# Optimization experiments

Hardware: AMD Instinct MI355X
Metric: run time of the kernel (lower is better)

Reference implementation:

```python
import jax, jax.numpy as jnp
import numpy as np

VOCAB, ED, HW, HS, NC = 100000, 200, 100, 100, 10
B, S, W = 128, 40, 50


def setup_inputs() -> dict:
    key = jax.random.key(0)
    ks = jax.random.split(key, 24)
    def p(k, shape, s=0.05):
        return jax.random.normal(k, shape, dtype=jnp.float32) * s
    emb = p(ks[0], (VOCAB, ED)).at[VOCAB - 1].set(0.0)  # padding_idx = vocab-1
    d = dict(
        x=jax.random.randint(ks[23], (B, S, W), 0, VOCAB),
        emb=emb,
        # word bidirectional GRU (forward + backward cells), torch gate order r,z,n
        w_Wih_f=p(ks[1], (3 * HW, ED)), w_bih_f=p(ks[2], (3 * HW,)), w_bhh_f=p(ks[3], (3 * HW,)),
        w_Wih_b=p(ks[4], (3 * HW, ED)), w_bih_b=p(ks[5], (3 * HW,)), w_bhh_b=p(ks[6], (3 * HW,)),
        # word attention
        wa_W=p(ks[7], (2 * HW, 2 * HW)), wa_b=p(ks[8], (2 * HW,)), wa_ctx=p(ks[9], (2 * HW,)),
        # sentence bidirectional GRU (input = 2*HW)
        s_Wih_f=p(ks[10], (3 * HS, 2 * HW)), s_bih_f=p(ks[11], (3 * HS,)), s_bhh_f=p(ks[12], (3 * HS,)),
        s_Wih_b=p(ks[13], (3 * HS, 2 * HW)), s_bih_b=p(ks[14], (3 * HS,)), s_bhh_b=p(ks[15], (3 * HS,)),
        # sentence attention
        sa_W=p(ks[16], (2 * HS, 2 * HS)), sa_b=p(ks[17], (2 * HS,)), sa_ctx=p(ks[18], (2 * HS,)),
        # classifier
        fc_W=p(ks[19], (NC, 2 * HS)), fc_b=p(ks[20], (NC,)),
    )
    return d


def _gru0(x, Wih, bih, bhh, H):
    # GRU cell from zero hidden state: W_hh @ h0 == 0, only b_hh survives.
    g = x @ Wih.T + bih  # [..., 3H], gate order r, z, n
    r = jax.nn.sigmoid(g[..., :H] + bhh[:H])
    z = jax.nn.sigmoid(g[..., H:2 * H] + bhh[H:2 * H])
    n = jnp.tanh(g[..., 2 * H:] + r * bhh[2 * H:])
    return (1.0 - z) * n  # h' = (1-z)*n + z*0


def _bigru0(x, Wf, bf, bhf, Wb, bb, bhb, H):
    # one-timestep bidirectional GRU: fwd and bwd cells both see zero state
    return jnp.concatenate([_gru0(x, Wf, bf, bhf, H), _gru0(x, Wb, bb, bhb, H)], axis=-1)


def _attn(x, Wa, ba, ctx):
    # additive attention pooling over the second-to-last axis
    scores = jnp.einsum('...nd,d->...n', jnp.tanh(x @ Wa.T + ba), ctx)
    alpha = jax.nn.softmax(scores, axis=-1)
    return jnp.einsum('...n,...nd->...d', alpha, x)


def reference(x, emb, w_Wih_f, w_bih_f, w_bhh_f, w_Wih_b, w_bih_b, w_bhh_b,
              wa_W, wa_b, wa_ctx, s_Wih_f, s_bih_f, s_bhh_f, s_Wih_b, s_bih_b, s_bhh_b,
              sa_W, sa_b, sa_ctx, fc_W, fc_b):
    e = emb[x]                                                   # [B,S,W,ED]
    wenc = _bigru0(e, w_Wih_f, w_bih_f, w_bhh_f, w_Wih_b, w_bih_b, w_bhh_b, HW)  # [B,S,W,2HW]
    svec = _attn(wenc, wa_W, wa_b, wa_ctx)                       # [B,S,2HW]
    senc = _bigru0(svec, s_Wih_f, s_bih_f, s_bhh_f, s_Wih_b, s_bih_b, s_bhh_b, HS)  # [B,S,2HS]
    dvec = _attn(senc, sa_W, sa_b, sa_ctx)                       # [B,2HS]
    logits = dvec @ fc_W.T + fc_b                                # [B,NC]
    return jax.nn.log_softmax(logits, axis=1)
```

## Files before the change

### kernel.cpp

```cpp
#include <hip/hip_runtime.h>
#include <math.h>

#define NB    128
#define NS    40
#define NW    50
#define ED    200
#define NHW   100
#define FEAT  200
#define NC    10
#define VOCABM1 99999
#define KL2E  1.4426950408889634f

#define BBn      19712ull
#define OFF_SV   846336ull
#define OFF_DV   2894336ull
#define WS_NEED  4194304ull

#define SLOT   19712

typedef short bf16x8 __attribute__((ext_vector_type(8)));
typedef float f32x4  __attribute__((ext_vector_type(4)));
typedef unsigned u32x4 __attribute__((ext_vector_type(4)));

__device__ __forceinline__ unsigned short f2bf(float f) {
    unsigned int u = __float_as_uint(f);
    u += 0x7fffu + ((u >> 16) & 1u);
    return (unsigned short)(u >> 16);
}
__device__ __forceinline__ float bf2f(short s) {
    return __uint_as_float(((unsigned int)(unsigned short)s) << 16);
}
__device__ __forceinline__ unsigned pk2(float a, float b) {
    return (unsigned)f2bf(a) | ((unsigned)f2bf(b) << 16);
}
__device__ __forceinline__ float frcp(float x) { return __builtin_amdgcn_rcpf(x); }
#if __has_builtin(__builtin_amdgcn_exp2f)
__device__ __forceinline__ float fexp2(float x){ return __builtin_amdgcn_exp2f(x); }
#else
__device__ __forceinline__ float fexp2(float x){ return exp2f(x); }
#endif
__device__ __forceinline__ float fsig(float x) { return frcp(1.f + __expf(-x)); }
__device__ __forceinline__ float ftanh(float x){ return 1.f - 2.f*frcp(1.f + __expf(2.f*x)); }

__device__ __forceinline__ unsigned cvtpk(float lo, float hi) {
    unsigned r;
    asm("v_cvt_pk_bf16_f32 %0, %1, %2" : "=v"(r) : "v"(lo), "v"(hi));
    return r;
}
__device__ __forceinline__ bf16x8 pack8(float4 a, float4 b) {
    u32x4 t;
    t[0] = cvtpk(a.x, a.y); t[1] = cvtpk(a.z, a.w);
    t[2] = cvtpk(b.x, b.y); t[3] = cvtpk(b.z, b.w);
    return __builtin_bit_cast(bf16x8, t);
}

__device__ __forceinline__ void gld16(const void* g, void* l) {
    __builtin_amdgcn_global_load_lds(
        (const __attribute__((address_space(1))) void*)g,
        (__attribute__((address_space(3))) void*)l, 16, 0, 0);
}

__device__ __forceinline__ void stageBlob(char* __restrict__ dst,
                                          const char* __restrict__ src, int tid)
{
    #pragma unroll
    for (int u = 0; u < 4; ++u)
        gld16(src + (size_t)(u * 256 + tid) * 16, dst + (size_t)(u * 256 + tid) * 16);
    if (tid < 208)
        gld16(src + (size_t)(1024 + tid) * 16, dst + (size_t)(1024 + tid) * 16);
}

__global__ void pack_kernel(
    const float* __restrict__ wWf, const float* __restrict__ wbif, const float* __restrict__ wbhf,
    const float* __restrict__ wWb, const float* __restrict__ wbib, const float* __restrict__ wbhb,
    const float* __restrict__ waW, const float* __restrict__ wab, const float* __restrict__ wactx,
    const float* __restrict__ sWf, const float* __restrict__ sbif, const float* __restrict__ sbhf,
    const float* __restrict__ sWb, const float* __restrict__ sbib, const float* __restrict__ sbhb,
    const float* __restrict__ saW, const float* __restrict__ sab, const float* __restrict__ sactx,
    char* __restrict__ ws)
{
    const int b = blockIdx.x, tid = threadIdx.x;
    const bool word = b < 19;
    const int lb = word ? b : b - 19;
    char* blob = ws + (size_t)b * BBn;

    if (lb < 14) {
        const int s = lb;
        const float* Wf_ = word ? wWf : sWf;
        const float* Wb_ = word ? wWb : sWb;
        const float* bif = word ? wbif : sbif;
        const float* bhf = word ? wbhf : sbhf;
        const float* bib = word ? wbib : sbib;
        const float* bhb = word ? wbhb : sbhb;
        const int ub = (s >> 1) * 32 + (s & 1) * 4;

        for (int e = tid; e < 18 * 64; e += 256) {
            const int f = e >> 6, l = e & 63;
            const int gate = f % 3, kk = f / 3;
            const int i = l & 15;
            const int k0 = kk * 32 + (l >> 4) * 8;
            const int u = ub + ((i >> 2) << 3) + (i & 3);
            u32x4 out = {0u, 0u, 0u, 0u};
            if (u < 200) {
                const float* W = (u < 100) ? Wf_ : Wb_;
                const int j = (u < 100) ? u : u - 100;
                const float* src = W + (size_t)(gate * NHW + j) * ED + k0;
                out[0] = pk2(src[0], src[1]); out[1] = pk2(src[2], src[3]);
                out[2] = pk2(src[4], src[5]); out[3] = pk2(src[6], src[7]);
            }
            *(u32x4*)(blob + ((size_t)f << 10) + (size_t)l * 16) = out;
        }
        if (tid < 48) {
            const int gate = tid >> 4, i = tid & 15;
            const int u = ub + ((i >> 2) << 3) + (i & 3);
            u32x4 out = {0u, 0u, 0u, 0u};
            if (u < 200) {
                const float* W = (u < 100) ? Wf_ : Wb_;
                const int j = (u < 100) ? u : u - 100;
                const float* src = W + (size_t)(gate * NHW + j) * ED + 192;
                out[0] = pk2(src[0], src[1]); out[1] = pk2(src[2], src[3]);
                out[2] = pk2(src[4], src[5]); out[3] = pk2(src[6], src[7]);
            }
            *(u32x4*)(blob + 18432 + gate * 256 + i * 16) = out;
        }
        if (tid < 64) {
            const int sect = tid >> 4, i = tid & 15;
            const int u = ub + ((i >> 2) << 3) + (i & 3);
            float v = 0.f;
            if (u < 200) {
                const float* bih = (u < 100) ? bif : bib;
                const float* bhh = (u < 100) ? bhf : bhb;
                const int j = (u < 100) ? u : u - 100;
                if (sect == 0)      v = -KL2E * (bih[j] + bhh[j]);
                else if (sect == 1) v =  KL2E * (bih[NHW + j] + bhh[NHW + j]);
                else if (sect == 2) v = 2.f * KL2E * bih[2 * NHW + j];
                else                v = 2.f * KL2E * bhh[2 * NHW + j];
            }
            *(float*)(blob + 19200 + sect * 64 + i * 4) = v;
        }
    } else {
        const int cb = lb - 14;
        const float* W  = word ? waW : saW;
        const float* ab = word ? wab : sab;
        const float* cx = word ? wactx : sactx;
        for (int e = tid; e < 18 * 64; e += 256) {
            const int f = e >> 6, l = e & 63;
            const int g = f % 3, kk = f / 3;
            const int d = cb * 48 + g * 16 + (l & 15);
            const int k0 = kk * 32 + (l >> 4) * 8;
            u32x4 out = {0u, 0u, 0u, 0u};
            if (d < FEAT) {
                const float* src = W + (size_t)d * FEAT + k0;
                out[0] = pk2(src[0], src[1]); out[1] = pk2(src[2], src[3]);
                out[2] = pk2(src[4], src[5]); out[3] = pk2(src[6], src[7]);
            }
            *(u32x4*)(blob + ((size_t)f << 10) + (size_t)l * 16) = out;
        }
        if (tid < 48) {
            const int g = tid >> 4, i = tid & 15;
            const int d = cb * 48 + g * 16 + i;
            u32x4 out = {0u, 0u, 0u, 0u};
            if (d < FEAT) {
                const float* src = W + (size_t)d * FEAT + 192;
                out[0] = pk2(src[0], src[1]); out[1] = pk2(src[2], src[3]);
                out[2] = pk2(src[4], src[5]); out[3] = pk2(src[6], src[7]);
            }
            *(u32x4*)(blob + 18432 + g * 256 + i * 16) = out;
        }
        if (tid < 48) {
            const int d = cb * 48 + tid;
            float ab2 = 0.f, cxn = 0.f;
            if (d < FEAT) { ab2 = 2.f * KL2E * ab[d]; cxn = -2.f * cx[d]; }
            *(float*)(blob + 19200 + tid * 4) = ab2;
            *(float*)(blob + 19392 + tid * 4) = cxn;
        }
    }
}

template<bool WORD>
__global__ __launch_bounds__(256, 3) void han_kernel(
    const int* __restrict__ xtok,
    const void* __restrict__ Ain,
    const char* __restrict__ pk,
    const int nvalid,
    unsigned short* __restrict__ Out)
{
    __shared__ __align__(16) char smem[2 * SLOT];
    char* bufs = smem;

    const int tid  = threadIdx.x;
    const int lane = tid & 63, wv = tid >> 6;
    const int grp  = wv >> 1, half = wv & 1;
    const int ln15 = lane & 15, q = lane >> 4;
    const long g   = (long)blockIdx.x * 2 + grp;
    float* sc_sh = (float*)(bufs + grp * 4096);
    float* al_sh = (float*)(bufs + grp * 4096 + 256);
    float* part  = (float*)(bufs + grp * 4096 + 512);

    stageBlob(bufs, pk, tid);

    bf16x8 af[2][7];
    if (WORD) {
        const float* emb = (const float*)Ain;
        #pragma unroll
        for (int Mt = 0; Mt < 2; ++Mt) {
            const int item = half * 32 + Mt * 16 + ln15;
            int tok = VOCABM1;
            if (item < nvalid) tok = xtok[g * nvalid + item];
            const float4* rp = (const float4*)(emb + (long)tok * ED);
            #pragma unroll
            for (int kc = 0; kc < 6; ++kc)
                af[Mt][kc] = pack8(rp[kc * 8 + q * 2], rp[kc * 8 + q * 2 + 1]);
            af[Mt][6] = (q == 0) ? pack8(rp[48], rp[49]) : (bf16x8)(short)0;
        }
    } else {
        const char* sv = (const char*)Ain;
        #pragma unroll
        for (int Mt = 0; Mt < 2; ++Mt) {
            const int item = half * 32 + Mt * 16 + ln15;
            const int ic = item < nvalid ? item : nvalid - 1;
            const char* rp = sv + (g * nvalid + ic) * 400;
            #pragma unroll
            for (int kc = 0; kc < 7; ++kc) {
                bf16x8 v = (bf16x8)(short)0;
                if (item < nvalid && (kc < 6 || q == 0))
                    v = *(const bf16x8*)(rp + kc * 64 + q * 16);
                af[Mt][kc] = v;
            }
        }
    }

    __syncthreads();

    u32x4 hfw[2][7];

    #pragma unroll
    for (int s = 0; s < 14; ++s) {
        stageBlob(bufs + (size_t)((s + 1) & 1) * SLOT, pk + (size_t)(s + 1) * BBn, tid);
        const char* cur = bufs + (size_t)(s & 1) * SLOT;

        f32x4 a0[2] = {}, a1[2] = {}, a2[2] = {};
        #pragma unroll
        for (int kk = 0; kk < 7; ++kk) {
            bf16x8 b0, b1, b2;
            if (kk < 6) {
                b0 = *(const bf16x8*)(cur + ((kk * 3 + 0) << 10) + lane * 16);
                b1 = *(const bf16x8*)(cur + ((kk * 3 + 1) << 10) + lane * 16);
                b2 = *(const bf16x8*)(cur + ((kk * 3 + 2) << 10) + lane * 16);
            } else {
                b0 = *(const bf16x8*)(cur + 18432 +   0 + ln15 * 16);
                b1 = *(const bf16x8*)(cur + 18432 + 256 + ln15 * 16);
                b2 = *(const bf16x8*)(cur + 18432 + 512 + ln15 * 16);
            }
            #pragma unroll
            for (int Mt = 0; Mt < 2; ++Mt) {
                a0[Mt] = __builtin_amdgcn_mfma_f32_16x16x32_bf16(b0, af[Mt][kk], a0[Mt], 0, 0, 0);
                a1[Mt] = __builtin_amdgcn_mfma_f32_16x16x32_bf16(b1, af[Mt][kk], a1[Mt], 0, 0, 0);
                a2[Mt] = __builtin_amdgcn_mfma_f32_16x16x32_bf16(b2, af[Mt][kk], a2[Mt], 0, 0, 0);
            }
        }
        const f32x4 bR = *(const f32x4*)(cur + 19200 +   0 + q * 16);
        const f32x4 bZ = *(const f32x4*)(cur + 19200 +  64 + q * 16);
        const f32x4 bN = *(const f32x4*)(cur + 19200 + 128 + q * 16);
        const f32x4 hN = *(const f32x4*)(cur + 19200 + 192 + q * 16);
        #pragma unroll
        for (int Mt = 0; Mt < 2; ++Mt) {
            float h[4];
            #pragma unroll
            for (int rg = 0; rg < 4; ++rg) {
                const float r  = frcp(1.f + fexp2(fmaf(a0[Mt][rg], -KL2E, bR[rg])));
                const float zc = frcp(1.f + fexp2(fmaf(a1[Mt][rg],  KL2E, bZ[rg])));
                const float t  = frcp(1.f + fexp2(fmaf(a2[Mt][rg], 2.f * KL2E,
                                          fmaf(r, hN[rg], bN[rg]))));
                h[rg] = zc * (1.f - 2.f * t);
            }
            hfw[Mt][s >> 1][(s & 1) * 2 + 0] = cvtpk(h[0], h[1]);
            hfw[Mt][s >> 1][(s & 1) * 2 + 1] = cvtpk(h[2], h[3]);
        }
        __syncthreads();
    }

    float sacc[2][4] = {{0.f}};
    #pragma unroll
    for (int s = 14; s < 19; ++s) {
        if (s + 1 < 19)
            stageBlob(bufs + (size_t)((s + 1) & 1) * SLOT, pk + (size_t)(s + 1) * BBn, tid);
        const char* cur = bufs + (size_t)(s & 1) * SLOT;

        f32x4 ac[2][3] = {};
        #pragma unroll
        for (int kk = 0; kk < 7; ++kk) {
            bf16x8 b0, b1, b2;
            if (kk < 6) {
                b0 = *(const bf16x8*)(cur + ((kk * 3 + 0) << 10) + lane * 16);
                b1 = *(const bf16x8*)(cur + ((kk * 3 + 1) << 10) + lane * 16);
                b2 = *(const bf16x8*)(cur + ((kk * 3 + 2) << 10) + lane * 16);
            } else {
                b0 = *(const bf16x8*)(cur + 18432 +   0 + ln15 * 16);
                b1 = *(const bf16x8*)(cur + 18432 + 256 + ln15 * 16);
                b2 = *(const bf16x8*)(cur + 18432 + 512 + ln15 * 16);
            }
            #pragma unroll
            for (int Mt = 0; Mt < 2; ++Mt) {
                const bf16x8 hfv = __builtin_bit_cast(bf16x8, hfw[Mt][kk]);
                ac[Mt][0] = __builtin_amdgcn_mfma_f32_16x16x32_bf16(hfv, b0, ac[Mt][0], 0, 0, 0);
                ac[Mt][1] = __builtin_amdgcn_mfma_f32_16x16x32_bf16(hfv, b1, ac[Mt][1], 0, 0, 0);
                ac[Mt][2] = __builtin_amdgcn_mfma_f32_16x16x32_bf16(hfv, b2, ac[Mt][2], 0, 0, 0);
            }
        }
        #pragma unroll
        for (int Nt = 0; Nt < 3; ++Nt) {
            const float ab2 = *(const float*)(cur + 19200 + (Nt * 16 + ln15) * 4);
            const float cxn = *(const float*)(cur + 19392 + (Nt * 16 + ln15) * 4);
            #pragma unroll
            for (int Mt = 0; Mt < 2; ++Mt)
                #pragma unroll
                for (int rg = 0; rg < 4; ++rg) {
                    const float u = frcp(1.f + fexp2(fmaf(ac[Mt][Nt][rg], 2.f * KL2E, ab2)));
                    sacc[Mt][rg] = fmaf(u, cxn, sacc[Mt][rg]);
                }
        }
        __syncthreads();
    }

    #pragma unroll
    for (int Mt = 0; Mt < 2; ++Mt)
        #pragma unroll
        for (int rg = 0; rg < 4; ++rg) {
            float v = sacc[Mt][rg];
            v += __shfl_xor(v, 1); v += __shfl_xor(v, 2);
            v += __shfl_xor(v, 4); v += __shfl_xor(v, 8);
            sacc[Mt][rg] = v;
        }
    if (ln15 == 0) {
        #pragma unroll
        for (int Mt = 0; Mt < 2; ++Mt)
            #pragma unroll
            for (int rg = 0; rg < 4; ++rg)
                sc_sh[half * 32 + Mt * 16 + q * 4 + rg] = sacc[Mt][rg];
    }
    __syncthreads();

    {
        const float sv0 = (lane < nvalid) ? sc_sh[lane] : -1e30f;
        float m = sv0;
        m = fmaxf(m, __shfl_xor(m, 1));  m = fmaxf(m, __shfl_xor(m, 2));
        m = fmaxf(m, __shfl_xor(m, 4));  m = fmaxf(m, __shfl_xor(m, 8));
        m = fmaxf(m, __shfl_xor(m, 16)); m = fmaxf(m, __shfl_xor(m, 32));
        const float e = (lane < nvalid) ? fexp2((sv0 - m) * KL2E) : 0.f;
        float ss = e;
        ss += __shfl_xor(ss, 1);  ss += __shfl_xor(ss, 2);
        ss += __shfl_xor(ss, 4);  ss += __shfl_xor(ss, 8);
        ss += __shfl_xor(ss, 16); ss += __shfl_xor(ss, 32);
        if (half == 0) al_sh[lane] = e * frcp(ss);
    }
    __syncthreads();

    {
        const float aM0 = al_sh[half * 32 + ln15];
        const float aM1 = al_sh[half * 32 + 16 + ln15];
        #pragma unroll
        for (int kc = 0; kc < 7; ++kc) {
            const bf16x8 h0 = __builtin_bit_cast(bf16x8, hfw[0][kc]);
            const bf16x8 h1 = __builtin_bit_cast(bf16x8, hfw[1][kc]);
            float p[8];
            #pragma unroll
            for (int j = 0; j < 8; ++j)
                p[j] = aM0 * bf2f(h0[j]) + aM1 * bf2f(h1[j]);
            #pragma unroll
            for (int j = 0; j < 8; ++j) {
                p[j] += __shfl_xor(p[j], 1); p[j] += __shfl_xor(p[j], 2);
                p[j] += __shfl_xor(p[j], 4); p[j] += __shfl_xor(p[j], 8);
            }
            if (ln15 == 0) {
                float* dst = part + (size_t)half * 224 + kc * 32 + q * 8;
                f32x4 v0 = {p[0], p[1], p[2], p[3]};
                f32x4 v1 = {p[4], p[5], p[6], p[7]};
                *(f32x4*)dst = v0; *(f32x4*)(dst + 4) = v1;
            }
        }
    }
    __syncthreads();

    if (tid < 100) {
        const int sl = tid / 50, i = tid - sl * 50;
        const float* pa = (const float*)(bufs + (size_t)sl * 4096 + 512);
        const float* pb = pa + 224;
        uint2 o;
        o.x = cvtpk(pa[i * 4 + 0] + pb[i * 4 + 0], pa[i * 4 + 1] + pb[i * 4 + 1]);
        o.y = cvtpk(pa[i * 4 + 2] + pb[i * 4 + 2], pa[i * 4 + 3] + pb[i * 4 + 3]);
        *(uint2*)(Out + ((long)blockIdx.x * 2 + sl) * 200 + i * 4) = o;
    }
}

__global__ void cls_kernel(const unsigned short* __restrict__ dvec,
                           const float* __restrict__ fcW, const float* __restrict__ fcb,
                           float* __restrict__ out)
{
    const int doc = blockIdx.x, lane = threadIdx.x;
    const int c = lane & 15, part = lane >> 4;
    const int cs = (c < NC) ? c : 0;
    float acc = (part == 0 && c < NC) ? fcb[c] : 0.f;
    for (int i = 0; i < 50; ++i) {
        const int k = part * 50 + i;
        const float a = bf2f((short)dvec[(size_t)doc * 200 + k]);
        acc += a * ((c < NC) ? fcW[(size_t)cs * 200 + k] : 0.f);
    }
    acc += __shfl_xor(acc, 16); acc += __shfl_xor(acc, 32);
    const float lg = (c < NC) ? acc : -1e30f;
    float m = lg;
    m = fmaxf(m, __shfl_xor(m, 1)); m = fmaxf(m, __shfl_xor(m, 2));
    m = fmaxf(m, __shfl_xor(m, 4)); m = fmaxf(m, __shfl_xor(m, 8));
    const float e = (c < NC) ? __expf(lg - m) : 0.f;
    float ss = e;
    ss += __shfl_xor(ss, 1); ss += __shfl_xor(ss, 2);
    ss += __shfl_xor(ss, 4); ss += __shfl_xor(ss, 8);
    const float lse = m + __logf(ss);
    if (lane < NC) out[(size_t)doc * NC + lane] = lg - lse;
}

template<int NWRD, int WT>
__device__ __forceinline__ void encode_block(
    float* __restrict__ e_sh, float* __restrict__ h_sh, float* __restrict__ sc_sh,
    const float* __restrict__ Wf, const float* __restrict__ bihf, const float* __restrict__ bhhf,
    const float* __restrict__ Wb, const float* __restrict__ bihb, const float* __restrict__ bhhb,
    const float* __restrict__ aW, const float* __restrict__ ab, const float* __restrict__ actx,
    int tid)
{
    constexpr int WG = NWRD / WT;
    for (int item = tid; item < FEAT * WG; item += 256) {
        const int unit = item % FEAT, wg = item / FEAT;
        const int dir = unit / NHW, j = unit - dir * NHW;
        const float* Wd  = dir ? Wb : Wf;
        const float* bih = dir ? bihb : bihf;
        const float* bhh = dir ? bhhb : bhhf;
        const float4* rowR = (const float4*)(Wd + (size_t)j * ED);
        const float4* rowZ = (const float4*)(Wd + (size_t)(NHW + j) * ED);
        const float4* rowN = (const float4*)(Wd + (size_t)(2 * NHW + j) * ED);
        float aR[WT], aZ[WT], aN[WT];
        #pragma unroll
        for (int t = 0; t < WT; ++t) { aR[t] = 0.f; aZ[t] = 0.f; aN[t] = 0.f; }
        const int w0 = wg * WT;
        #pragma unroll 1
        for (int k4 = 0; k4 < ED / 4; ++k4) {
            const float4 wr = rowR[k4], wz = rowZ[k4], wn = rowN[k4];
            #pragma unroll
            for (int t = 0; t < WT; ++t) {
                const float4 e = *(const float4*)(e_sh + (w0 + t) * ED + k4 * 4);
                aR[t] += wr.x*e.x + wr.y*e.y + wr.z*e.z + wr.w*e.w;
                aZ[t] += wz.x*e.x + wz.y*e.y + wz.z*e.z + wz.w*e.w;
                aN[t] += wn.x*e.x + wn.y*e.y + wn.z*e.z + wn.w*e.w;
            }
        }
        const float bR = bih[j] + bhh[j], bZ = bih[NHW+j] + bhh[NHW+j];
        const float bN = bih[2*NHW+j], hN = bhh[2*NHW+j];
        #pragma unroll
        for (int t = 0; t < WT; ++t) {
            const float r = fsig(aR[t] + bR), z = fsig(aZ[t] + bZ);
            const float n = ftanh(aN[t] + bN + r * hN);
            h_sh[(w0 + t) * FEAT + unit] = (1.f - z) * n;
        }
    }
    __syncthreads();
    for (int item = tid; item < FEAT * WG; item += 256) {
        const int d = item % FEAT, wg = item / FEAT;
        const float4* row = (const float4*)(aW + (size_t)d * FEAT);
        float acc[WT];
        #pragma unroll
        for (int t = 0; t < WT; ++t) acc[t] = 0.f;
        const int w0 = wg * WT;
        #pragma unroll 1
        for (int k4 = 0; k4 < FEAT / 4; ++k4) {
            const float4 wv = row[k4];
            #pragma unroll
            for (int t = 0; t < WT; ++t) {
                const float4 h = *(const float4*)(h_sh + (w0 + t) * FEAT + k4 * 4);
                acc[t] += wv.x*h.x + wv.y*h.y + wv.z*h.z + wv.w*h.w;
            }
        }
        const float bb = ab[d], cc = actx[d];
        #pragma unroll
        for (int t = 0; t < WT; ++t)
            e_sh[d * NWRD + (w0 + t)] = ftanh(acc[t] + bb) * cc;
    }
    __syncthreads();
    if (tid < NWRD) {
        float s = 0.f;
        for (int d = 0; d < FEAT; ++d) s += e_sh[d * NWRD + tid];
        sc_sh[tid] = s;
    }
    __syncthreads();
    if (tid == 0) {
        float m = -1e30f;
        for (int w = 0; w < NWRD; ++w) m = fmaxf(m, sc_sh[w]);
        float s = 0.f;
        for (int w = 0; w < NWRD; ++w) { const float ev = __expf(sc_sh[w] - m); sc_sh[w] = ev; s += ev; }
        const float inv = 1.f / s;
        for (int w = 0; w < NWRD; ++w) sc_sh[w] *= inv;
    }
    __syncthreads();
}

__global__ __launch_bounds__(256) void word_kernel_f32(
    const int* __restrict__ x, const float* __restrict__ emb,
    const float* __restrict__ Wf, const float* __restrict__ bihf, const float* __restrict__ bhhf,
    const float* __restrict__ Wb, const float* __restrict__ bihb, const float* __restrict__ bhhb,
    const float* __restrict__ waW, const float* __restrict__ wab, const float* __restrict__ wactx,
    float* __restrict__ svec)
{
    __shared__ __align__(16) float e_sh[NW * ED];
    __shared__ __align__(16) float h_sh[NW * FEAT];
    __shared__ float sc_sh[NW];
    const int sent = blockIdx.x, tid = threadIdx.x;
    const int* xr = x + (size_t)sent * NW;
    for (int i = tid * 4; i < NW * ED; i += 256 * 4) {
        const int w = i / ED, k = i - w * ED;
        *(float4*)(e_sh + i) = *(const float4*)(emb + (size_t)xr[w] * ED + k);
    }
    __syncthreads();
    encode_block<NW, 25>(e_sh, h_sh, sc_sh, Wf, bihf, bhhf, Wb, bihb, bhhb, waW, wab, wactx, tid);
    if (tid < FEAT) {
        float a = 0.f;
        #pragma unroll 1
        for (int w = 0; w < NW; ++w) a += sc_sh[w] * h_sh[w * FEAT + tid];
        svec[(size_t)sent * FEAT + tid] = a;
    }
}

__global__ __launch_bounds__(256) void sent_kernel_f32(
    const float* __restrict__ svec,
    const float* __restrict__ Wf, const float* __restrict__ bihf, const float* __restrict__ bhhf,
    const float* __restrict__ Wb, const float* __restrict__ bihb, const float* __restrict__ bhhb,
    const float* __restrict__ saW, const float* __restrict__ sab, const float* __restrict__ sactx,
    const float* __restrict__ fcW, const float* __restrict__ fcb,
    float* __restrict__ out)
{
    __shared__ __align__(16) float e_sh[NS * ED];
    __shared__ __align__(16) float h_sh[NS * FEAT];
    __shared__ float sc_sh[NS];
    __shared__ float dvec_sh[FEAT];
    __shared__ float logit_sh[NC];
    __shared__ float lse_sh;
    const int b = blockIdx.x, tid = threadIdx.x;
    const float* src = svec + (size_t)b * NS * FEAT;
    for (int i = tid * 4; i < NS * FEAT; i += 256 * 4)
        *(float4*)(e_sh + i) = *(const float4*)(src + i);
    __syncthreads();
    encode_block<NS, 20>(e_sh, h_sh, sc_sh, Wf, bihf, bhhf, Wb, bihb, bhhb, saW, sab, sactx, tid);
    if (tid < FEAT) {
        float a = 0.f;
        #pragma unroll 1
        for (int s = 0; s < NS; ++s) a += sc_sh[s] * h_sh[s * FEAT + tid];
        dvec_sh[tid] = a;
    }
    __syncthreads();
    if (tid < NC) {
        float a = fcb[tid];
        const float* row = fcW + (size_t)tid * FEAT;
        for (int k = 0; k < FEAT; ++k) a += row[k] * dvec_sh[k];
        logit_sh[tid] = a;
    }
    __syncthreads();
    if (tid == 0) {
        float m = -1e30f;
        for (int c = 0; c < NC; ++c) m = fmaxf(m, logit_sh[c]);
        float s = 0.f;
        for (int c = 0; c < NC; ++c) s += __expf(logit_sh[c] - m);
        lse_sh = m + logf(s);
    }
    __syncthreads();
    if (tid < NC) out[(size_t)b * NC + tid] = logit_sh[tid] - lse_sh;
}

extern "C" void kernel_launch(void* const* d_in, const int* in_sizes, int n_in,
                              void* d_out, int out_size, void* d_ws, size_t ws_size,
                              hipStream_t stream)
{
    const int*   x     = (const int*)d_in[0];
    const float* emb   = (const float*)d_in[1];
    const float* wWf   = (const float*)d_in[2];
    const float* wbif  = (const float*)d_in[3];
    const float* wbhf  = (const float*)d_in[4];
    const float* wWb   = (const float*)d_in[5];
    const float* wbib  = (const float*)d_in[6];
    const float* wbhb  = (const float*)d_in[7];
    const float* waW   = (const float*)d_in[8];
    const float* wab   = (const float*)d_in[9];
    const float* wactx = (const float*)d_in[10];
    const float* sWf   = (const float*)d_in[11];
    const float* sbif  = (const float*)d_in[12];
    const float* sbhf  = (const float*)d_in[13];
    const float* sWb   = (const float*)d_in[14];
    const float* sbib  = (const float*)d_in[15];
    const float* sbhb  = (const float*)d_in[16];
    const float* saW   = (const float*)d_in[17];
    const float* sab   = (const float*)d_in[18];
    const float* sactx = (const float*)d_in[19];
    const float* fcW   = (const float*)d_in[20];
    const float* fcb   = (const float*)d_in[21];
    float* out = (float*)d_out;

    if (ws_size < WS_NEED) {
        float* svec = (float*)d_ws;
        word_kernel_f32<<<NB * NS, 256, 0, stream>>>(
            x, emb, wWf, wbif, wbhf, wWb, wbib, wbhb, waW, wab, wactx, svec);
        sent_kernel_f32<<<NB, 256, 0, stream>>>(
            svec, sWf, sbif, sbhf, sWb, sbib, sbhb, saW, sab, sactx, fcW, fcb, out);
        return;
    }

    char* ws = (char*)d_ws;
    unsigned short* svec = (unsigned short*)(ws + OFF_SV);
    unsigned short* dvec = (unsigned short*)(ws + OFF_DV);

    pack_kernel<<<38, 256, 0, stream>>>(
        wWf, wbif, wbhf, wWb, wbib, wbhb, waW, wab, wactx,
        sWf, sbif, sbhf, sWb, sbib, sbhb, saW, sab, sactx, ws);

    han_kernel<true><<<NB * NS / 2, 256, 0, stream>>>(
        x, emb, ws, NW, svec);

    han_kernel<false><<<NB / 2, 256, 0, stream>>>(
        nullptr, svec, ws + 19ull * BBn, NS, dvec);

    cls_kernel<<<NB, 64, 0, stream>>>(dvec, fcW, fcb, out);
}
```

Baseline: 337.4 us.

## Run sentence kernel with one document per block; raise word kernel occupancy hint

Templates the HAN kernel on the number of documents per block so the sentence-level pass launches 128 blocks of 128 threads instead of 64 blocks of 256, spreading its work across more CUs. The blob staging loop is generalised to 128 threads. The word-level kernel's launch_bounds min-blocks rises from 3 to 4, which lowers the register cap and may cause spills in exchange for higher occupancy.

```diff
diff --git a/kernel.cpp b/kernel.cpp
--- a/kernel.cpp
+++ b/kernel.cpp
@@ -60,14 +60,23 @@
         (__attribute__((address_space(3))) void*)l, 16, 0, 0);
 }
 
+template<int NTHR>
 __device__ __forceinline__ void stageBlob(char* __restrict__ dst,
                                           const char* __restrict__ src, int tid)
 {
-    #pragma unroll
-    for (int u = 0; u < 4; ++u)
-        gld16(src + (size_t)(u * 256 + tid) * 16, dst + (size_t)(u * 256 + tid) * 16);
-    if (tid < 208)
-        gld16(src + (size_t)(1024 + tid) * 16, dst + (size_t)(1024 + tid) * 16);
+    if constexpr (NTHR == 256) {
+        #pragma unroll
+        for (int u = 0; u < 4; ++u)
+            gld16(src + (size_t)(u * 256 + tid) * 16, dst + (size_t)(u * 256 + tid) * 16);
+        if (tid < 208)
+            gld16(src + (size_t)(1024 + tid) * 16, dst + (size_t)(1024 + tid) * 16);
+    } else {
+        #pragma unroll
+        for (int u = 0; u < 9; ++u)
+            gld16(src + (size_t)(u * 128 + tid) * 16, dst + (size_t)(u * 128 + tid) * 16);
+        if (tid < 80)
+            gld16(src + (size_t)(1152 + tid) * 16, dst + (size_t)(1152 + tid) * 16);
+    }
 }
 
 __global__ void pack_kernel(
@@ -177,8 +186,8 @@
     }
 }
 
-template<bool WORD>
-__global__ __launch_bounds__(256, 3) void han_kernel(
+template<bool WORD, int NG>
+__global__ __launch_bounds__(NG * 128, NG == 2 ? 4 : 2) void han_kernel(
     const int* __restrict__ xtok,
     const void* __restrict__ Ain,
     const char* __restrict__ pk,
@@ -190,14 +199,15 @@
 
     const int tid  = threadIdx.x;
     const int lane = tid & 63, wv = tid >> 6;
-    const int grp  = wv >> 1, half = wv & 1;
+    const int grp  = (NG == 2) ? (wv >> 1) : 0;
+    const int half = (NG == 2) ? (wv & 1) : wv;
     const int ln15 = lane & 15, q = lane >> 4;
-    const long g   = (long)blockIdx.x * 2 + grp;
+    const long g   = (long)blockIdx.x * NG + grp;
     float* sc_sh = (float*)(bufs + grp * 4096);
     float* al_sh = (float*)(bufs + grp * 4096 + 256);
     float* part  = (float*)(bufs + grp * 4096 + 512);
 
-    stageBlob(bufs, pk, tid);
+    stageBlob<NG * 128>(bufs, pk, tid);
 
     bf16x8 af[2][7];
     if (WORD) {
@@ -236,7 +246,8 @@
 
     #pragma unroll
     for (int s = 0; s < 14; ++s) {
-        stageBlob(bufs + (size_t)((s + 1) & 1) * SLOT, pk + (size_t)(s + 1) * BBn, tid);
+        stageBlob<NG * 128>(bufs + (size_t)((s + 1) & 1) * SLOT,
+                            pk + (size_t)(s + 1) * BBn, tid);
         const char* cur = bufs + (size_t)(s & 1) * SLOT;
 
         f32x4 a0[2] = {}, a1[2] = {}, a2[2] = {};
@@ -284,7 +295,8 @@
     #pragma unroll
     for (int s = 14; s < 19; ++s) {
         if (s + 1 < 19)
-            stageBlob(bufs + (size_t)((s + 1) & 1) * SLOT, pk + (size_t)(s + 1) * BBn, tid);
+            stageBlob<NG * 128>(bufs + (size_t)((s + 1) & 1) * SLOT,
+                                pk + (size_t)(s + 1) * BBn, tid);
         const char* cur = bufs + (size_t)(s & 1) * SLOT;
 
         f32x4 ac[2][3] = {};
@@ -382,14 +394,14 @@
     }
     __syncthreads();
 
-    if (tid < 100) {
+    if (tid < NG * 50) {
         const int sl = tid / 50, i = tid - sl * 50;
         const float* pa = (const float*)(bufs + (size_t)sl * 4096 + 512);
         const float* pb = pa + 224;
         uint2 o;
         o.x = cvtpk(pa[i * 4 + 0] + pb[i * 4 + 0], pa[i * 4 + 1] + pb[i * 4 + 1]);
         o.y = cvtpk(pa[i * 4 + 2] + pb[i * 4 + 2], pa[i * 4 + 3] + pb[i * 4 + 3]);
-        *(uint2*)(Out + ((long)blockIdx.x * 2 + sl) * 200 + i * 4) = o;
+        *(uint2*)(Out + ((long)blockIdx.x * NG + sl) * 200 + i * 4) = o;
     }
 }
 
@@ -617,10 +629,10 @@
         wWf, wbif, wbhf, wWb, wbib, wbhb, waW, wab, wactx,
         sWf, sbif, sbhf, sWb, sbib, sbhb, saW, sab, sactx, ws);
 
-    han_kernel<true><<<NB * NS / 2, 256, 0, stream>>>(
+    han_kernel<true, 2><<<NB * NS / 2, 256, 0, stream>>>(
         x, emb, ws, NW, svec);
 
-    han_kernel<false><<<NB / 2, 256, 0, stream>>>(
+    han_kernel<false, 1><<<NB, 128, 0, stream>>>(
         nullptr, svec, ws + 19ull * BBn, NS, dvec);
 
     cls_kernel<<<NB, 64, 0, stream>>>(dvec, fcW, fcb, out);
```

Result: slower. 366.3 us (+8.5%).
